# Kernel tuning notes

Hardware: AMD Instinct MI355X
Metric: run time of the kernel (lower is better)

Reference implementation:

```python
import jax, jax.numpy as jnp
import numpy as np

ENC_D, PRED_D, JOINT_D, VOCAB = 256, 256, 512, 1024

def setup_inputs() -> dict:
    key = jax.random.key(0)
    ks = jax.random.split(key, 8)
    B, T, U = 4, 256, 64
    s = lambda d: 1.0 / np.sqrt(d)
    return {
        "encoder_outputs": jax.random.normal(ks[0], (B, T, ENC_D), jnp.float32),
        "predictor_outputs": jax.random.normal(ks[1], (B, U, PRED_D), jnp.float32),
        "W_enc": jax.random.uniform(ks[2], (ENC_D, JOINT_D), jnp.float32, -s(ENC_D), s(ENC_D)),
        "b_enc": jax.random.uniform(ks[3], (JOINT_D,), jnp.float32, -s(ENC_D), s(ENC_D)),
        "W_dec": jax.random.uniform(ks[4], (PRED_D, JOINT_D), jnp.float32, -s(PRED_D), s(PRED_D)),
        "b_dec": jax.random.uniform(ks[5], (JOINT_D,), jnp.float32, -s(PRED_D), s(PRED_D)),
        "W_out": jax.random.uniform(ks[6], (JOINT_D, VOCAB), jnp.float32, -s(JOINT_D), s(JOINT_D)),
        "b_out": jax.random.uniform(ks[7], (VOCAB,), jnp.float32, -s(JOINT_D), s(JOINT_D)),
    }

def reference(encoder_outputs, predictor_outputs, W_enc, b_enc, W_dec, b_dec, W_out, b_out):
    # [B,T,J] and [B,U,J] projections
    enc = jnp.einsum('bte,ej->btj', encoder_outputs, W_enc) + b_enc
    pred = jnp.einsum('bup,pj->buj', predictor_outputs, W_dec) + b_dec
    # broadcast add -> [B,T,U,J], tanh, then output projection -> [B,T,U,V]
    joint = jnp.tanh(enc[:, :, None, :] + pred[:, None, :, :])
    logits = jnp.einsum('btuj,jv->btuv', joint, W_out) + b_out
    return logits
```

## Files before the change

### kernel.cpp

```cpp
#include <hip/hip_runtime.h>
#include <hip/hip_bf16.h>

typedef __attribute__((ext_vector_type(8))) short bf16x8;
typedef __attribute__((ext_vector_type(4))) float f32x4;
typedef __attribute__((ext_vector_type(4))) float fvec4;
typedef __attribute__((ext_vector_type(8))) unsigned short u16x8;


__device__ __forceinline__ unsigned short f2bf(float f) {
  unsigned int u = __builtin_bit_cast(unsigned int, f);
  u += 0x7FFFu + ((u >> 16) & 1u);
  return (unsigned short)(u >> 16);
}

__device__ __forceinline__ float fast_tanh(float x) {
  float cx = fminf(fmaxf(x, -9.0f), 9.0f);
  float e2 = __expf(cx + cx);
  return (e2 - 1.0f) * __builtin_amdgcn_rcpf(e2 + 1.0f);
}


__device__ __forceinline__ void proj_body(
    const float* __restrict__ x, const float* __restrict__ W,
    const float* __restrict__ bias, float* __restrict__ out,
    int blk, uint8_t* sh) {
  float (*xt)[9] = (float (*)[9])sh;
  const int tid = threadIdx.x;
  const int row0 = blk << 3;
  #pragma unroll
  for (int i = 0; i < 8; ++i)
    xt[tid][i] = x[(size_t)(row0 + i) * 256 + tid];
  __syncthreads();
  float acc0[8] = {0.f,0.f,0.f,0.f,0.f,0.f,0.f,0.f};
  float acc1[8] = {0.f,0.f,0.f,0.f,0.f,0.f,0.f,0.f};
  #pragma unroll 4
  for (int k = 0; k < 256; ++k) {
    float w0 = W[(size_t)k * 512 + tid];
    float w1 = W[(size_t)k * 512 + tid + 256];
    #pragma unroll
    for (int r = 0; r < 8; ++r) {
      float xv = xt[k][r];
      acc0[r] = fmaf(xv, w0, acc0[r]);
      acc1[r] = fmaf(xv, w1, acc1[r]);
    }
  }
  float b0 = bias[tid], b1 = bias[tid + 256];
  #pragma unroll
  for (int r = 0; r < 8; ++r) {
    out[(size_t)(row0 + r) * 512 + tid]       = acc0[r] + b0;
    out[(size_t)(row0 + r) * 512 + tid + 256] = acc1[r] + b1;
  }
}

__device__ __forceinline__ void transpose_body(
    const float* __restrict__ W, unsigned short* __restrict__ Bt2,
    int blk, uint8_t* sh) {
  unsigned short (*tile)[65] = (unsigned short (*)[65])sh;
  const int k0 = (blk & 7) << 6;
  const int n0 = (blk >> 3) << 6;
  const int tid = threadIdx.x;
  #pragma unroll
  for (int i = 0; i < 16; ++i) {
    int idx = tid + (i << 8);
    int r = idx >> 6, c = idx & 63;
    tile[r][c] = f2bf(W[(size_t)(k0 + r) * 1024 + n0 + c]);
  }
  __syncthreads();
  #pragma unroll
  for (int i = 0; i < 16; ++i) {
    int idx = tid + (i << 8);
    int r = idx >> 6, c = idx & 63;
    int ng = n0 + r, kg = k0 + c;
    size_t dst = ((size_t)(ng >> 9) << 18) + ((size_t)(kg >> 5) << 14)
               + ((ng & 511) << 5) + (kg & 31);
    Bt2[dst] = tile[c][r];
  }
}

__global__ __launch_bounds__(256) void prep_kernel(
    const float* __restrict__ enc, const float* __restrict__ We,
    const float* __restrict__ be, float* __restrict__ encp,
    const float* __restrict__ pred, const float* __restrict__ Wd,
    const float* __restrict__ bd, float* __restrict__ predp,
    const float* __restrict__ Wo, unsigned short* __restrict__ Bt2) {
  __shared__ uint8_t sh[9216];
  const int b = blockIdx.x;
  if (b < 128)       proj_body(enc, We, be, encp, b, sh);
  else if (b < 160)  proj_body(pred, Wd, bd, predp, b - 128, sh);
  else               transpose_body(Wo, Bt2, b - 160, sh);
}

__global__ __launch_bounds__(512, 4) void fused_gemm(
    const float* __restrict__ encp, const float* __restrict__ predp,
    const unsigned short* __restrict__ Bt2, const float* __restrict__ bout,
    float* __restrict__ out) {
  __shared__ uint8_t Alds[65536];
  const int tid = threadIdx.x;
  const int lane = tid & 63, wid = tid >> 6;
  const int fr = lane & 15, fg = lane >> 4;
  const int b = blockIdx.x;
  const int wg = ((b & 7) << 8) + (b >> 3);
  const int mt = wg >> 1, half = wg & 1;
  const int m0 = mt << 6;
  const int cb0 = half << 9;

  const unsigned short* Bgl =
      Bt2 + ((size_t)half << 18) + (((wid << 6) + fr) << 5) + (fg << 3);

  bf16x8 bA[4], bB[4];
  #pragma unroll
  for (int nf = 0; nf < 4; ++nf)
    bA[nf] = *(const bf16x8*)(Bgl + (nf << 9));

  {
    const int r = tid >> 3, cb = tid & 7;
    const float* erow = encp + ((size_t)mt << 9);
    const float* prow = predp + ((size_t)(((mt >> 8) << 6) + r) << 9);
    uint8_t* rowbase = Alds + (r << 10);
    #pragma unroll
    for (int c8 = 0; c8 < 8; ++c8) {
      int chunk = cb + (c8 << 3);
      int k8 = chunk << 3;
      fvec4 e0 = *(const fvec4*)(erow + k8);
      fvec4 e1 = *(const fvec4*)(erow + k8 + 4);
      fvec4 p0 = *(const fvec4*)(prow + k8);
      fvec4 p1 = *(const fvec4*)(prow + k8 + 4);
      u16x8 o;
      #pragma unroll
      for (int i = 0; i < 4; ++i) o[i]     = f2bf(fast_tanh(e0[i] + p0[i]));
      #pragma unroll
      for (int i = 0; i < 4; ++i) o[i + 4] = f2bf(fast_tanh(e1[i] + p1[i]));
      *(u16x8*)(rowbase + ((chunk ^ (r & 7)) << 4)) = o;
    }
  }
  __syncthreads();

  f32x4 acc[4][4];
  f32x4 zero4 = {0.f, 0.f, 0.f, 0.f};
  #pragma unroll
  for (int i = 0; i < 4; ++i)
    #pragma unroll
    for (int j = 0; j < 4; ++j) acc[i][j] = zero4;

  const int qh = (fr >> 2) & 1;
  int arow[4];
  #pragma unroll
  for (int mf = 0; mf < 4; ++mf)
    arow[mf] = ((((mf << 4) + fr)) << 10) + ((fg ^ (fr & 3)) << 4);

  auto step = [&](int kt, bf16x8 (&cur)[4], bf16x8 (&nxt)[4]) {
    const int ktn = kt < 15 ? kt + 1 : 15;
    #pragma unroll
    for (int nf = 0; nf < 4; ++nf)
      nxt[nf] = *(const bf16x8*)(Bgl + (ktn << 14) + (nf << 9));
    const int ko = (kt ^ qh) << 6;
    bf16x8 af[4];
    #pragma unroll
    for (int mf = 0; mf < 4; ++mf)
      af[mf] = *(const bf16x8*)(Alds + arow[mf] + ko);
    #pragma unroll
    for (int mf = 0; mf < 4; ++mf)
      #pragma unroll
      for (int nf = 0; nf < 4; ++nf)
        acc[mf][nf] = __builtin_amdgcn_mfma_f32_16x16x32_bf16(cur[nf], af[mf],
                                                              acc[mf][nf], 0, 0, 0);
  };

  #pragma unroll
  for (int kt = 0; kt < 16; kt += 2) {
    step(kt,     bA, bB);
    step(kt + 1, bB, bA);
  }

  float (*epi)[516] = (float (*)[516])Alds;
  const int colw = (wid << 6) + (fg << 2);
  fvec4 bvv[4];
  #pragma unroll
  for (int nf = 0; nf < 4; ++nf)
    bvv[nf] = *(const fvec4*)&bout[cb0 + colw + (nf << 4)];

  #pragma unroll
  for (int mf = 0; mf < 4; ++mf) {
    __syncthreads();
    #pragma unroll
    for (int nf = 0; nf < 4; ++nf) {
      fvec4 o = acc[mf][nf] + bvv[nf];
      *(fvec4*)&epi[fr][colw + (nf << 4)] = o;
    }
    __syncthreads();
    #pragma unroll
    for (int j = 0; j < 4; ++j) {
      const int idx = (wid << 2) + j;
      const int row = idx >> 1, seg = idx & 1;
      fvec4 v = *(const fvec4*)&epi[row][(seg << 8) + (lane << 2)];
      __builtin_nontemporal_store(
          v, (fvec4*)&out[(size_t)(m0 + (mf << 4) + row) * 1024 + cb0 +
                          (seg << 8) + (lane << 2)]);
    }
  }
}

extern "C" void kernel_launch(void* const* d_in, const int* in_sizes, int n_in,
                              void* d_out, int out_size, void* d_ws, size_t ws_size,
                              hipStream_t stream) {
  const float* enc   = (const float*)d_in[0];
  const float* pred  = (const float*)d_in[1];
  const float* W_enc = (const float*)d_in[2];
  const float* b_enc = (const float*)d_in[3];
  const float* W_dec = (const float*)d_in[4];
  const float* b_dec = (const float*)d_in[5];
  const float* W_out = (const float*)d_in[6];
  const float* b_out = (const float*)d_in[7];
  float* out = (float*)d_out;

  uint8_t* ws = (uint8_t*)d_ws;
  float* encp  = (float*)ws;
  float* predp = (float*)(ws + 2097152);
  unsigned short* bt2 = (unsigned short*)(ws + 2621440);

  prep_kernel<<<288, 256, 0, stream>>>(enc, W_enc, b_enc, encp,
                                       pred, W_dec, b_dec, predp,
                                       W_out, bt2);
  fused_gemm<<<2048, 512, 0, stream>>>(encp, predp, bt2, b_out, out);
}
```

Measured before the change: 125.0 us.

## Enlarge GEMM tile to 256x256 with 16 waves and K-split A build

Each workgroup now covers a 256-row by 256-column output tile with 1024 threads (4x4 waves) instead of 64x512 with 512 threads. The tanh-joint A tile is built in two K halves that reuse a single LDS region, and the epilogue alternates between two LDS staging buffers. The goal is more reuse of B fragments across M and fewer redundant A builds per output column. The cost is a large LDS footprint (about 130 KB), which likely caps occupancy at one workgroup per CU, plus extra barriers around the mid-K rebuild of A.

```diff
diff --git a/kernel.cpp b/kernel.cpp
--- a/kernel.cpp
+++ b/kernel.cpp
@@ -90,36 +90,38 @@
   else               transpose_body(Wo, Bt2, b - 160, sh);
 }
 
-__global__ __launch_bounds__(512, 4) void fused_gemm(
+__global__ __launch_bounds__(1024, 4) void fused_gemm(
     const float* __restrict__ encp, const float* __restrict__ predp,
     const unsigned short* __restrict__ Bt2, const float* __restrict__ bout,
     float* __restrict__ out) {
-  __shared__ uint8_t Alds[65536];
+  __shared__ uint8_t lds[133120];
   const int tid = threadIdx.x;
   const int lane = tid & 63, wid = tid >> 6;
   const int fr = lane & 15, fg = lane >> 4;
+  const int wm = wid >> 2, wn = wid & 3;
   const int b = blockIdx.x;
-  const int wg = ((b & 7) << 8) + (b >> 3);
-  const int mt = wg >> 1, half = wg & 1;
-  const int m0 = mt << 6;
-  const int cb0 = half << 9;
+  const int wg = ((b & 7) << 7) + (b >> 3);
+  const int nq = wg >> 8, mt = wg & 255;
+  const int m0 = mt << 8;
+  const int n0 = nq << 8;
 
   const unsigned short* Bgl =
-      Bt2 + ((size_t)half << 18) + (((wid << 6) + fr) << 5) + (fg << 3);
+      Bt2 + ((size_t)(nq >> 1) << 18) +
+      ((((nq & 1) << 8) + (wn << 6) + fr) << 5) + (fg << 3);
 
   bf16x8 bA[4], bB[4];
   #pragma unroll
   for (int nf = 0; nf < 4; ++nf)
     bA[nf] = *(const bf16x8*)(Bgl + (nf << 9));
 
-  {
-    const int r = tid >> 3, cb = tid & 7;
-    const float* erow = encp + ((size_t)mt << 9);
-    const float* prow = predp + ((size_t)(((mt >> 8) << 6) + r) << 9);
-    uint8_t* rowbase = Alds + (r << 10);
+  auto build_A = [&](int kp) {
+    const int r = tid >> 2, cb = tid & 3;
+    const float* erow = encp + (((size_t)(mt << 2) + (r >> 6)) << 9) + (kp << 8);
+    const float* prow = predp + (((size_t)((mt >> 6) << 6) + (r & 63)) << 9) + (kp << 8);
+    uint8_t* rowbase = lds + (r << 9);
     #pragma unroll
     for (int c8 = 0; c8 < 8; ++c8) {
-      int chunk = cb + (c8 << 3);
+      int chunk = cb + (c8 << 2);
       int k8 = chunk << 3;
       fvec4 e0 = *(const fvec4*)(erow + k8);
       fvec4 e1 = *(const fvec4*)(erow + k8 + 4);
@@ -132,8 +134,11 @@
       for (int i = 0; i < 4; ++i) o[i + 4] = f2bf(fast_tanh(e1[i] + p1[i]));
       *(u16x8*)(rowbase + ((chunk ^ (r & 7)) << 4)) = o;
     }
-  }
-  __syncthreads();
+  };
+
+  build_A(0);
+  asm volatile("s_waitcnt lgkmcnt(0)" ::: "memory");
+  __builtin_amdgcn_s_barrier();
 
   f32x4 acc[4][4];
   f32x4 zero4 = {0.f, 0.f, 0.f, 0.f};
@@ -146,18 +151,18 @@
   int arow[4];
   #pragma unroll
   for (int mf = 0; mf < 4; ++mf)
-    arow[mf] = ((((mf << 4) + fr)) << 10) + ((fg ^ (fr & 3)) << 4);
+    arow[mf] = (((wm << 6) + (mf << 4) + fr) << 9) + ((fg ^ (fr & 3)) << 4);
 
   auto step = [&](int kt, bf16x8 (&cur)[4], bf16x8 (&nxt)[4]) {
     const int ktn = kt < 15 ? kt + 1 : 15;
     #pragma unroll
     for (int nf = 0; nf < 4; ++nf)
-      nxt[nf] = *(const bf16x8*)(Bgl + (ktn << 14) + (nf << 9));
-    const int ko = (kt ^ qh) << 6;
+      nxt[nf] = *(const bf16x8*)(Bgl + ((size_t)ktn << 14) + (nf << 9));
+    const int ko = ((kt & 7) ^ qh) << 6;
     bf16x8 af[4];
     #pragma unroll
     for (int mf = 0; mf < 4; ++mf)
-      af[mf] = *(const bf16x8*)(Alds + arow[mf] + ko);
+      af[mf] = *(const bf16x8*)(lds + arow[mf] + ko);
     #pragma unroll
     for (int mf = 0; mf < 4; ++mf)
       #pragma unroll
@@ -167,35 +172,47 @@
   };
 
   #pragma unroll
-  for (int kt = 0; kt < 16; kt += 2) {
+  for (int kt = 0; kt < 8; kt += 2) {
     step(kt,     bA, bB);
     step(kt + 1, bB, bA);
   }
-
-  float (*epi)[516] = (float (*)[516])Alds;
-  const int colw = (wid << 6) + (fg << 2);
+  asm volatile("s_waitcnt lgkmcnt(0)" ::: "memory");
+  __builtin_amdgcn_s_barrier();
+  build_A(1);
+  asm volatile("s_waitcnt lgkmcnt(0)" ::: "memory");
+  __builtin_amdgcn_s_barrier();
+  #pragma unroll
+  for (int kt = 8; kt < 16; kt += 2) {
+    step(kt,     bA, bB);
+    step(kt + 1, bB, bA);
+  }
+
+  const int colw = (wn << 6) + (fg << 2);
   fvec4 bvv[4];
   #pragma unroll
   for (int nf = 0; nf < 4; ++nf)
-    bvv[nf] = *(const fvec4*)&bout[cb0 + colw + (nf << 4)];
-
+    bvv[nf] = *(const fvec4*)&bout[n0 + colw + (nf << 4)];
+
+  const int er_dep = (wm << 4) + fr;
   #pragma unroll
   for (int mf = 0; mf < 4; ++mf) {
-    __syncthreads();
+    float* ep = (float*)(lds + (mf & 1) * 66560);
+    asm volatile("s_waitcnt lgkmcnt(0)" ::: "memory");
+    __builtin_amdgcn_s_barrier();
     #pragma unroll
     for (int nf = 0; nf < 4; ++nf) {
       fvec4 o = acc[mf][nf] + bvv[nf];
-      *(fvec4*)&epi[fr][colw + (nf << 4)] = o;
-    }
-    __syncthreads();
+      *(fvec4*)&ep[er_dep * 260 + colw + (nf << 4)] = o;
+    }
+    asm volatile("s_waitcnt lgkmcnt(0)" ::: "memory");
+    __builtin_amdgcn_s_barrier();
     #pragma unroll
     for (int j = 0; j < 4; ++j) {
-      const int idx = (wid << 2) + j;
-      const int row = idx >> 1, seg = idx & 1;
-      fvec4 v = *(const fvec4*)&epi[row][(seg << 8) + (lane << 2)];
+      const int er = (wid << 2) + j;
+      fvec4 v = *(const fvec4*)&ep[er * 260 + (lane << 2)];
+      const int gm = m0 + ((er >> 4) << 6) + (mf << 4) + (er & 15);
       __builtin_nontemporal_store(
-          v, (fvec4*)&out[(size_t)(m0 + (mf << 4) + row) * 1024 + cb0 +
-                          (seg << 8) + (lane << 2)]);
+          v, (fvec4*)&out[(size_t)gm * 1024 + n0 + (lane << 2)]);
     }
   }
 }
@@ -221,5 +238,5 @@
   prep_kernel<<<288, 256, 0, stream>>>(enc, W_enc, b_enc, encp,
                                        pred, W_dec, b_dec, predp,
                                        W_out, bt2);
-  fused_gemm<<<2048, 512, 0, stream>>>(encp, predp, bt2, b_out, out);
-}
+  fused_gemm<<<1024, 1024, 0, stream>>>(encp, predp, bt2, b_out, out);
+}
```

Measured after the change: 225.7 us. 80.5% more time.
